# Kernel optimization log

Hardware: AMD Instinct MI355X
Metric: run time of the kernel (lower is better)

## Reference

```python
import jax, jax.numpy as jnp
import numpy as np

N_NODES = 4096
HID = 64
N_STEP = 10
_OFFSETS = np.array([1, 2, 5, 11, 23, 47, 97, 193])  # circulant graph -> degree 16


def setup_inputs() -> dict:
    rng = np.random.default_rng(0)
    N = N_NODES
    i = np.repeat(np.arange(N), len(_OFFSETS))
    j = (i + np.tile(_OFFSETS, N)) % N
    vals = rng.normal(0.0, 0.5, i.shape).astype(np.float32)
    J = np.zeros((N, N), np.float32)
    J[i, j] = vals
    J[j, i] = vals  # symmetric coupling matrix
    row, col = np.nonzero(J)                      # E directed edges, row-major sorted
    key_fwd = row.astype(np.int64) * N + col
    rev = np.searchsorted(key_fwd, col.astype(np.int64) * N + row)  # reverse-edge index
    ru, cu = np.nonzero(np.triu(J))               # Eu upper-triangular edges
    u2e = np.searchsorted(key_fwd, ru.astype(np.int64) * N + cu)    # upper -> full edge index
    bias = rng.normal(0.0, 0.5, N).astype(np.float32)
    p = lambda *s: jnp.asarray(rng.normal(0.0, 0.1, s).astype(np.float32))
    return {
        'J': jnp.asarray(J), 'bias': jnp.asarray(bias),
        'gat_W': p(4, HID), 'gat_a': p(2 * HID, 1),
        'ci_W1': p(4, HID), 'ci_b1': jnp.zeros((HID,), jnp.float32),
        'ci_W2': p(HID, HID), 'ci_b2': jnp.zeros((HID,), jnp.float32),
        'ci_W3': p(HID, 1), 'ci_b3': jnp.zeros((1,), jnp.float32),
        'row': jnp.asarray(row.astype(np.int32)), 'col': jnp.asarray(col.astype(np.int32)),
        'rev': jnp.asarray(rev.astype(np.int32)),
        'ru': jnp.asarray(ru.astype(np.int32)), 'cu': jnp.asarray(cu.astype(np.int32)),
        'u2e': jnp.asarray(u2e.astype(np.int32)),
        'N_step': N_STEP, 'MPNNtype': 0,
    }


def reference(J, bias, gat_W, gat_a, ci_W1, ci_b1, ci_W2, ci_b2, ci_W3, ci_b3,
              row, col, rev, ru, cu, u2e, N_step, MPNNtype):
    N = J.shape[0]
    adj = (jnp.abs(J) > 0).astype(J.dtype)
    # node features: [-b, b, degree, row-sum of J]
    feat = jnp.stack([-bias, bias, adj.sum(1), J.sum(1)], axis=1)  # [N,4]
    # GAT scores: e[i,j] = leakyrelu([Wh_i || Wh_j] @ a) = leakyrelu(Wh_i@a1 + Wh_j@a2)
    Wh = feat @ gat_W                                  # [N,H]
    f1 = Wh @ gat_a[:HID, 0]
    f2 = Wh @ gat_a[HID:, 0]
    e = jax.nn.leaky_relu(f1[:, None] + f2[None, :], 0.2)
    att = jnp.where(adj > 0, jnp.exp(e), 0.0)
    Cij_matrix = 0.5 * (att + att.T)                   # [N,N]
    Cij_e = Cij_matrix[row, col]                       # [E]
    # Ci readout MLP
    h = jax.nn.relu(feat @ ci_W1 + ci_b1)
    h = jax.nn.relu(h @ ci_W2 + ci_b2)
    Ci = h @ ci_W3 + ci_b3                             # [N,1]
    dom = Ci + Cij_matrix.sum(1, keepdims=True)
    dom = jnp.sign(dom) * jnp.maximum(jnp.abs(dom), 0.1)  # clamp |.| >= 0.1
    bias_scale = bias / dom[:, 0]
    bx_scale = jnp.stack([-bias_scale, bias_scale], axis=1)  # [N,2]
    Jv = J[row, col]
    Jxy_scale = jnp.stack([jnp.stack([Jv, -Jv], -1),
                           jnp.stack([-Jv, Jv], -1)], axis=1) / Cij_e[:, None, None]  # [E,2,2]

    def node_update(em):
        # node_messages[j,:] = sum over edges (i->j) of em[e,:]
        nm = jax.ops.segment_sum(em, col, num_segments=N) / dom   # [N,2]
        lnZ = jnp.log(jnp.sum(jnp.exp(bx_scale + nm), axis=1, keepdims=True))
        return bx_scale + nm - lnZ, lnZ

    em0 = jnp.zeros((row.shape[0], 2), J.dtype)  # log of all-ones messages
    hidden0, lnZ0 = node_update(em0)

    def bp_step(carry, _):
        em, hidden, lnZ = carry
        ln_pj = hidden[row][:, :, None]     # [E,2,1]
        ln_zj = lnZ[row][:, :, None]        # [E,1,1]
        ln_mu_ij = em[rev][:, :, None]      # message on reverse edge, [E,2,1]
        M = jnp.exp(Jxy_scale + ln_pj + ln_zj - ln_mu_ij)          # [E,2,2]
        M = M / jnp.sum(jnp.max(M, axis=1), axis=1)[:, None, None]
        em_new = jnp.log(jnp.max(M ** Cij_e[:, None, None], axis=1))  # [E,2]
        hidden_new, lnZ_new = node_update(em_new)
        return (em_new, hidden_new, lnZ_new), None

    (em, hidden, lnZ), _ = jax.lax.scan(bp_step, (em0, hidden0, lnZ0), None, length=N_step)

    readout = jnp.exp(hidden)                           # [N,2]
    Js = J[ru, cu] / Cij_matrix[ru, cu]                 # [Eu]
    Jxy_u = jnp.exp(jnp.stack([jnp.stack([Js, -Js], -1),
                               jnp.stack([-Js, Js], -1)], axis=1))  # [Eu,2,2]
    temp_i = readout[cu] / jnp.exp(em[u2e])             # [Eu,2]
    temp_j = readout[ru] / jnp.exp(em[rev[u2e]])        # [Eu,2]
    pw = Jxy_u * temp_i[:, None, :] * temp_j[:, :, None]
    pw = pw / jnp.sum(pw, axis=(1, 2), keepdims=True)
    readout_pairwise = pw.reshape(-1, 4)                # [Eu,4]
    Cij_u = Cij_matrix[ru, cu]
    node_H = -jnp.sum(readout * jnp.log(readout + 1e-16), axis=1)
    edge_H = -jnp.sum(readout_pairwise * jnp.log(readout_pairwise + 1e-16), axis=1)
    node_entropy = Ci[:, 0] @ jax.lax.stop_gradient(node_H)
    edge_entropy = Cij_u @ jax.lax.stop_gradient(edge_H)
    return (readout, readout_pairwise, node_entropy + edge_entropy,
            node_entropy, edge_entropy, Ci[:, 0], Cij_u, dom)
```

## Files before the change

### kernel.cpp

```cpp
#include <hip/hip_runtime.h>
#include <cstddef>

#define TB    512
#define NB    128
#define NSTEP 10

__device__ __forceinline__ float lse2(float a, float b) {
    return fmaxf(a, b) + __logf(1.0f + __expf(-fabsf(a - b)));
}

__device__ __forceinline__ void stA(float2* p, float2 v) {
    union { float2 f; unsigned long long u; } x; x.f = v;
    __hip_atomic_store((unsigned long long*)p, x.u,
                       __ATOMIC_RELAXED, __HIP_MEMORY_SCOPE_AGENT);
}
__device__ __forceinline__ float2 ldA(const float2* p) {
    union { float2 f; unsigned long long u; } x;
    x.u = __hip_atomic_load((const unsigned long long*)p,
                            __ATOMIC_RELAXED, __HIP_MEMORY_SCOPE_AGENT);
    return x.f;
}

struct KParams {
    const float *J, *bias, *gat_W, *gat_a, *W1, *b1, *W2, *b2, *W3, *b3;
    const int *col, *rev, *ru, *cu, *u2e;
    int N, Eu;
    float2 *jsC, *uA, *uB, *em;
    int*    bar;
    float  *ci_out, *dom_out, *ent;
    float2* ro_out;
    float4* rp_out;
    float*  cij_out;
};

__device__ __forceinline__ void grid_bar(int* flags, int expect) {
    __syncthreads();
    if (threadIdx.x == 0)
        __hip_atomic_store(&flags[blockIdx.x * 32], expect,
                           __ATOMIC_RELAXED, __HIP_MEMORY_SCOPE_AGENT);
    if (threadIdx.x < NB) {
        while (__hip_atomic_load(&flags[threadIdx.x * 32], __ATOMIC_RELAXED,
                                 __HIP_MEMORY_SCOPE_AGENT) < expect) {}
    }
    __syncthreads();
}

__global__ __launch_bounds__(TB) void k_fused(KParams p) {
    __shared__ float sW2[64 * 64];
    __shared__ float sh1[TB / 16][65];
    __shared__ float red[TB / 64];

    const int tidb = threadIdx.x;
    const int g = blockIdx.x * TB + tidb;
    const int i = g >> 4, t = g & 15;
    const int lane = tidb & 63;

    for (int k = tidb; k < 64 * 64; k += TB) sW2[k] = p.W2[k];
    if (g < 3) {
        __hip_atomic_store((int*)&p.ent[g], 0,
                           __ATOMIC_RELAXED, __HIP_MEMORY_SCOPE_AGENT);
    }

    const int j  = p.col[g];
    const float Jv = p.J[(size_t)i * (size_t)p.N + (size_t)j];

    float rs = Jv;
    rs += __shfl_xor(rs, 1); rs += __shfl_xor(rs, 2);
    rs += __shfl_xor(rs, 4); rs += __shfl_xor(rs, 8);

    float rsj = 0.0f;
    {
        const int* colj = p.col + 16 * j;
        const float* Jrow = p.J + (size_t)j * (size_t)p.N;
        #pragma unroll 4
        for (int tt = 0; tt < 16; ++tt) rsj += Jrow[colj[tt]];
    }

    const float bi = p.bias[i], bj = p.bias[j];

    float s8 = 0.0f;
    if (lane < 8) {
        int k = lane & 3;
        const float* a = p.gat_a + ((lane < 4) ? 0 : 64);
        for (int h = 0; h < 64; ++h) s8 += p.gat_W[k * 64 + h] * a[h];
    }
    const float w10 = __shfl(s8, 0), w11 = __shfl(s8, 1), w12 = __shfl(s8, 2), w13 = __shfl(s8, 3);
    const float w20 = __shfl(s8, 4), w21 = __shfl(s8, 5), w22 = __shfl(s8, 6), w23 = __shfl(s8, 7);
    const float fd = 16.0f;
    const float f1i = -bi * w10 + bi * w11 + fd * w12 + rs  * w13;
    const float f2i = -bi * w20 + bi * w21 + fd * w22 + rs  * w23;
    const float f1j = -bj * w10 + bj * w11 + fd * w12 + rsj * w13;
    const float f2j = -bj * w20 + bj * w21 + fd * w22 + rsj * w23;

    float x1 = f1i + f2j; x1 = (x1 > 0.0f) ? x1 : 0.2f * x1;
    float x2 = f1j + f2i; x2 = (x2 > 0.0f) ? x2 : 0.2f * x2;
    const float C  = 0.5f * (__expf(x1) + __expf(x2));
    const float js = Jv / C;
    stA(&p.jsC[g], make_float2(js, C));

    float sc = C;
    sc += __shfl_xor(sc, 1); sc += __shfl_xor(sc, 2);
    sc += __shfl_xor(sc, 4); sc += __shfl_xor(sc, 8);

    const int nib = tidb >> 4;
    __syncthreads();
    #pragma unroll
    for (int m = 0; m < 4; ++m) {
        int h = t + 16 * m;
        float a = -bi * p.W1[h] + bi * p.W1[64 + h] + fd * p.W1[128 + h]
                + rs * p.W1[192 + h] + p.b1[h];
        sh1[nib][h] = fmaxf(a, 0.0f);
    }
    __syncthreads();
    float civ = 0.0f;
    #pragma unroll
    for (int m = 0; m < 4; ++m) {
        int o = t + 16 * m;
        float acc = p.b2[o];
        for (int h = 0; h < 64; ++h) acc += sh1[nib][h] * sW2[h * 64 + o];
        civ += fmaxf(acc, 0.0f) * p.W3[o];
    }
    civ += __shfl_xor(civ, 1); civ += __shfl_xor(civ, 2);
    civ += __shfl_xor(civ, 4); civ += __shfl_xor(civ, 8);
    const float ci = civ + p.b3[0];

    const float s  = ci + sc;
    const float cl = fmaxf(fabsf(s), 0.1f);
    const float d  = (s > 0.0f) ? cl : ((s < 0.0f) ? -cl : 0.0f);
    const float rd = 1.0f / d;
    const float bs = bi * rd;
    if (t == 0) {
        p.ci_out[i] = ci;
        p.dom_out[i] = d;
        stA(&p.uA[i], make_float2(-bs, bs));
    }
    grid_bar(p.bar, 1);

    int eE = 0, eR = 0, eC = 0, eEr = 0;
    float jse = 0.0f, Ce = 0.0f;
    if (g < p.Eu) {
        eE = p.u2e[g]; eR = p.ru[g]; eC = p.cu[g];
        eEr = p.rev[eE];
        const float2 jc = ldA(&p.jsC[eE]);
        jse = jc.x; Ce = jc.y;
    }

    float in0 = 0.0f, in1 = 0.0f;
    float out0 = 0.0f, out1 = 0.0f;
    float ui0 = -bs, ui1 = bs;
    float2 *uP = p.uA, *uQ = p.uB;
    for (int st = 0; st < NSTEP; ++st) {
        const float2 uj = ldA(&uP[j]);
        const float a0 = uj.x - out0, a1 = uj.y - out1;
        const float t0 = fmaxf( js + a0, -js + a1);
        const float t1 = fmaxf(-js + a0,  js + a1);
        const float ls = lse2(t0, t1);
        const float ni0 = C * (t0 - ls), ni1 = C * (t1 - ls);
        const float b0 = ui0 - in0, b1 = ui1 - in1;
        const float q0 = fmaxf( js + b0, -js + b1);
        const float q1 = fmaxf(-js + b0,  js + b1);
        const float qs = lse2(q0, q1);
        out0 = C * (q0 - qs); out1 = C * (q1 - qs);
        in0 = ni0; in1 = ni1;

        float nm0 = in0, nm1 = in1;
        nm0 += __shfl_xor(nm0, 1); nm1 += __shfl_xor(nm1, 1);
        nm0 += __shfl_xor(nm0, 2); nm1 += __shfl_xor(nm1, 2);
        nm0 += __shfl_xor(nm0, 4); nm1 += __shfl_xor(nm1, 4);
        nm0 += __shfl_xor(nm0, 8); nm1 += __shfl_xor(nm1, 8);
        ui0 = -bs + nm0 * rd; ui1 = bs + nm1 * rd;
        if (t == 0) stA(&uQ[i], make_float2(ui0, ui1));

        if (st == NSTEP - 1) {
            stA(&p.em[g], make_float2(in0, in1));
            float nodeC = 0.0f;
            if (t == 0) {
                const float lz = lse2(ui0, ui1);
                const float r0 = __expf(ui0 - lz), r1 = __expf(ui1 - lz);
                p.ro_out[i] = make_float2(r0, r1);
                const float H = -(r0 * __logf(r0 + 1e-16f) + r1 * __logf(r1 + 1e-16f));
                nodeC = ci * H;
            }
            for (int off = 32; off > 0; off >>= 1) nodeC += __shfl_down(nodeC, off);
            const int wv = tidb >> 6;
            if (lane == 0) red[wv] = nodeC;
            __syncthreads();
            if (tidb == 0) {
                float sn = 0.0f;
                #pragma unroll
                for (int w = 0; w < TB / 64; ++w) sn += red[w];
                atomicAdd(&p.ent[0], sn);
                atomicAdd(&p.ent[1], sn);
            }
        }
        grid_bar(p.bar, 2 + st);
        float2* tp = uP; uP = uQ; uQ = tp;
    }

    float edgeC = 0.0f;
    if (g < p.Eu) {
        const float2 uc = ldA(&uP[eC]), ur = ldA(&uP[eR]);
        const float lc = lse2(uc.x, uc.y);
        const float lr = lse2(ur.x, ur.y);
        const float2 eme = ldA(&p.em[eEr]);
        const float2 emr = ldA(&p.em[eE]);
        const float ti0 = (uc.x - lc) - eme.x, ti1 = (uc.y - lc) - eme.y;
        const float tj0 = (ur.x - lr) - emr.x, tj1 = (ur.y - lr) - emr.y;
        const float L00 =  jse + ti0 + tj0;
        const float L01 = -jse + ti1 + tj0;
        const float L10 = -jse + ti0 + tj1;
        const float L11 =  jse + ti1 + tj1;
        const float mL = fmaxf(fmaxf(L00, L01), fmaxf(L10, L11));
        float p00 = __expf(L00 - mL), p01 = __expf(L01 - mL);
        float p10 = __expf(L10 - mL), p11 = __expf(L11 - mL);
        const float inv = 1.0f / (p00 + p01 + p10 + p11);
        p00 *= inv; p01 *= inv; p10 *= inv; p11 *= inv;
        p.rp_out[g] = make_float4(p00, p01, p10, p11);
        p.cij_out[g] = Ce;
        const float H = -(p00 * __logf(p00 + 1e-16f) + p01 * __logf(p01 + 1e-16f)
                        + p10 * __logf(p10 + 1e-16f) + p11 * __logf(p11 + 1e-16f));
        edgeC = Ce * H;
    }
    for (int off = 32; off > 0; off >>= 1) edgeC += __shfl_down(edgeC, off);
    const int wv = tidb >> 6;
    if (lane == 0) red[wv] = edgeC;
    __syncthreads();
    if (tidb == 0) {
        float se = 0.0f;
        #pragma unroll
        for (int w = 0; w < TB / 64; ++w) se += red[w];
        atomicAdd(&p.ent[0], se);
        atomicAdd(&p.ent[2], se);
    }
}

extern "C" void kernel_launch(void* const* d_in, const int* in_sizes, int n_in,
                              void* d_out, int out_size, void* d_ws, size_t ws_size,
                              hipStream_t stream) {
    const int N  = in_sizes[1];
    const int E  = in_sizes[10];
    const int Eu = in_sizes[13];

    float* out = (float*)d_out;
    size_t OFF_RP  = 2 * (size_t)N;
    size_t OFF_ENT = OFF_RP + 4 * (size_t)Eu;

    char* w = (char*)d_ws;
    auto carve = [&](size_t bytes) {
        void* q = (void*)w;
        w += (bytes + 255) & ~(size_t)255;
        return q;
    };

    KParams p;
    p.J     = (const float*)d_in[0];
    p.bias  = (const float*)d_in[1];
    p.gat_W = (const float*)d_in[2];
    p.gat_a = (const float*)d_in[3];
    p.W1    = (const float*)d_in[4];
    p.b1    = (const float*)d_in[5];
    p.W2    = (const float*)d_in[6];
    p.b2    = (const float*)d_in[7];
    p.W3    = (const float*)d_in[8];
    p.b3    = (const float*)d_in[9];
    p.col   = (const int*)d_in[11];
    p.rev   = (const int*)d_in[12];
    p.ru    = (const int*)d_in[13];
    p.cu    = (const int*)d_in[14];
    p.u2e   = (const int*)d_in[15];
    p.N = N; p.Eu = Eu;

    p.jsC   = (float2*)carve((size_t)E * 8);
    p.uA    = (float2*)carve((size_t)N * 8);
    p.uB    = (float2*)carve((size_t)N * 8);
    p.em    = (float2*)carve((size_t)E * 8);
    p.bar   = (int*)carve((size_t)NB * 128);

    p.ro_out  = (float2*)out;
    p.rp_out  = (float4*)(out + OFF_RP);
    p.ent     = out + OFF_ENT;
    p.ci_out  = p.ent + 3;
    p.cij_out = p.ci_out + N;
    p.dom_out = p.cij_out + Eu;

    hipMemsetAsync(p.bar, 0, (size_t)NB * 128, stream);
    k_fused<<<dim3(NB), dim3(TB), 0, stream>>>(p);
}
```

Baseline: 160.4 us.

## Replace grid barriers with per-value sentinel polling and step-indexed buffers

Drops the all-block grid barrier. Each value (node GAT features, jsC, em, per-step messages) is now written to a buffer prefilled with a sentinel (0xFF), and consumers spin until their specific entries become valid. Per-step message buffers are indexed by step so they are never overwritten, which removes the need for double buffering. Neighbour row-sum recomputation is replaced by reading the neighbour's published f1/f2. This adds a memset of about 11*N plus 2*E float2 per call and relies on relaxed atomics holding the ordering between data producers and polling consumers.

```diff
diff --git a/kernel.cpp b/kernel.cpp
--- a/kernel.cpp
+++ b/kernel.cpp
@@ -4,6 +4,7 @@
 #define TB    512
 #define NB    128
 #define NSTEP 10
+#define SENTV 0xFFFFFFFFFFFFFFFFULL
 
 __device__ __forceinline__ float lse2(float a, float b) {
     return fmaxf(a, b) + __logf(1.0f + __expf(-fabsf(a - b)));
@@ -14,10 +15,15 @@
     __hip_atomic_store((unsigned long long*)p, x.u,
                        __ATOMIC_RELAXED, __HIP_MEMORY_SCOPE_AGENT);
 }
-__device__ __forceinline__ float2 ldA(const float2* p) {
+__device__ __forceinline__ float2 pollLd(const float2* p) {
     union { float2 f; unsigned long long u; } x;
     x.u = __hip_atomic_load((const unsigned long long*)p,
                             __ATOMIC_RELAXED, __HIP_MEMORY_SCOPE_AGENT);
+    while (x.u == SENTV) {
+        __builtin_amdgcn_s_sleep(1);
+        x.u = __hip_atomic_load((const unsigned long long*)p,
+                                __ATOMIC_RELAXED, __HIP_MEMORY_SCOPE_AGENT);
+    }
     return x.f;
 }
 
@@ -25,26 +31,13 @@
     const float *J, *bias, *gat_W, *gat_a, *W1, *b1, *W2, *b2, *W3, *b3;
     const int *col, *rev, *ru, *cu, *u2e;
     int N, Eu;
-    float2 *jsC, *uA, *uB, *em;
-    int*    bar;
+    float2 *fA, *jsC, *em, *uS;
     float  *ci_out, *dom_out, *ent;
     float2* ro_out;
     float4* rp_out;
     float*  cij_out;
 };
 
-__device__ __forceinline__ void grid_bar(int* flags, int expect) {
-    __syncthreads();
-    if (threadIdx.x == 0)
-        __hip_atomic_store(&flags[blockIdx.x * 32], expect,
-                           __ATOMIC_RELAXED, __HIP_MEMORY_SCOPE_AGENT);
-    if (threadIdx.x < NB) {
-        while (__hip_atomic_load(&flags[threadIdx.x * 32], __ATOMIC_RELAXED,
-                                 __HIP_MEMORY_SCOPE_AGENT) < expect) {}
-    }
-    __syncthreads();
-}
-
 __global__ __launch_bounds__(TB) void k_fused(KParams p) {
     __shared__ float sW2[64 * 64];
     __shared__ float sh1[TB / 16][65];
@@ -54,6 +47,7 @@
     const int g = blockIdx.x * TB + tidb;
     const int i = g >> 4, t = g & 15;
     const int lane = tidb & 63;
+    const int N = p.N;
 
     for (int k = tidb; k < 64 * 64; k += TB) sW2[k] = p.W2[k];
     if (g < 3) {
@@ -62,21 +56,13 @@
     }
 
     const int j  = p.col[g];
-    const float Jv = p.J[(size_t)i * (size_t)p.N + (size_t)j];
+    const float Jv = p.J[(size_t)i * (size_t)N + (size_t)j];
 
     float rs = Jv;
     rs += __shfl_xor(rs, 1); rs += __shfl_xor(rs, 2);
     rs += __shfl_xor(rs, 4); rs += __shfl_xor(rs, 8);
 
-    float rsj = 0.0f;
-    {
-        const int* colj = p.col + 16 * j;
-        const float* Jrow = p.J + (size_t)j * (size_t)p.N;
-        #pragma unroll 4
-        for (int tt = 0; tt < 16; ++tt) rsj += Jrow[colj[tt]];
-    }
-
-    const float bi = p.bias[i], bj = p.bias[j];
+    const float bi = p.bias[i];
 
     float s8 = 0.0f;
     if (lane < 8) {
@@ -87,20 +73,9 @@
     const float w10 = __shfl(s8, 0), w11 = __shfl(s8, 1), w12 = __shfl(s8, 2), w13 = __shfl(s8, 3);
     const float w20 = __shfl(s8, 4), w21 = __shfl(s8, 5), w22 = __shfl(s8, 6), w23 = __shfl(s8, 7);
     const float fd = 16.0f;
-    const float f1i = -bi * w10 + bi * w11 + fd * w12 + rs  * w13;
-    const float f2i = -bi * w20 + bi * w21 + fd * w22 + rs  * w23;
-    const float f1j = -bj * w10 + bj * w11 + fd * w12 + rsj * w13;
-    const float f2j = -bj * w20 + bj * w21 + fd * w22 + rsj * w23;
-
-    float x1 = f1i + f2j; x1 = (x1 > 0.0f) ? x1 : 0.2f * x1;
-    float x2 = f1j + f2i; x2 = (x2 > 0.0f) ? x2 : 0.2f * x2;
-    const float C  = 0.5f * (__expf(x1) + __expf(x2));
-    const float js = Jv / C;
-    stA(&p.jsC[g], make_float2(js, C));
-
-    float sc = C;
-    sc += __shfl_xor(sc, 1); sc += __shfl_xor(sc, 2);
-    sc += __shfl_xor(sc, 4); sc += __shfl_xor(sc, 8);
+    const float f1i = -bi * w10 + bi * w11 + fd * w12 + rs * w13;
+    const float f2i = -bi * w20 + bi * w21 + fd * w22 + rs * w23;
+    if (t == 0) stA(&p.fA[i], make_float2(f1i, f2i));
 
     const int nib = tidb >> 4;
     __syncthreads();
@@ -124,6 +99,16 @@
     civ += __shfl_xor(civ, 4); civ += __shfl_xor(civ, 8);
     const float ci = civ + p.b3[0];
 
+    const float2 fj = pollLd(&p.fA[j]);
+    float x1 = f1i + fj.y; x1 = (x1 > 0.0f) ? x1 : 0.2f * x1;
+    float x2 = fj.x + f2i; x2 = (x2 > 0.0f) ? x2 : 0.2f * x2;
+    const float C  = 0.5f * (__expf(x1) + __expf(x2));
+    const float js = Jv / C;
+    stA(&p.jsC[g], make_float2(js, C));
+
+    float sc = C;
+    sc += __shfl_xor(sc, 1); sc += __shfl_xor(sc, 2);
+    sc += __shfl_xor(sc, 4); sc += __shfl_xor(sc, 8);
     const float s  = ci + sc;
     const float cl = fmaxf(fabsf(s), 0.1f);
     const float d  = (s > 0.0f) ? cl : ((s < 0.0f) ? -cl : 0.0f);
@@ -132,25 +117,20 @@
     if (t == 0) {
         p.ci_out[i] = ci;
         p.dom_out[i] = d;
-        stA(&p.uA[i], make_float2(-bs, bs));
-    }
-    grid_bar(p.bar, 1);
+        stA(&p.uS[i], make_float2(-bs, bs));
+    }
 
     int eE = 0, eR = 0, eC = 0, eEr = 0;
-    float jse = 0.0f, Ce = 0.0f;
     if (g < p.Eu) {
         eE = p.u2e[g]; eR = p.ru[g]; eC = p.cu[g];
         eEr = p.rev[eE];
-        const float2 jc = ldA(&p.jsC[eE]);
-        jse = jc.x; Ce = jc.y;
     }
 
     float in0 = 0.0f, in1 = 0.0f;
     float out0 = 0.0f, out1 = 0.0f;
     float ui0 = -bs, ui1 = bs;
-    float2 *uP = p.uA, *uQ = p.uB;
     for (int st = 0; st < NSTEP; ++st) {
-        const float2 uj = ldA(&uP[j]);
+        const float2 uj = pollLd(&p.uS[(size_t)st * N + j]);
         const float a0 = uj.x - out0, a1 = uj.y - out1;
         const float t0 = fmaxf( js + a0, -js + a1);
         const float t1 = fmaxf(-js + a0,  js + a1);
@@ -169,41 +149,43 @@
         nm0 += __shfl_xor(nm0, 4); nm1 += __shfl_xor(nm1, 4);
         nm0 += __shfl_xor(nm0, 8); nm1 += __shfl_xor(nm1, 8);
         ui0 = -bs + nm0 * rd; ui1 = bs + nm1 * rd;
-        if (t == 0) stA(&uQ[i], make_float2(ui0, ui1));
-
-        if (st == NSTEP - 1) {
-            stA(&p.em[g], make_float2(in0, in1));
-            float nodeC = 0.0f;
-            if (t == 0) {
-                const float lz = lse2(ui0, ui1);
-                const float r0 = __expf(ui0 - lz), r1 = __expf(ui1 - lz);
-                p.ro_out[i] = make_float2(r0, r1);
-                const float H = -(r0 * __logf(r0 + 1e-16f) + r1 * __logf(r1 + 1e-16f));
-                nodeC = ci * H;
-            }
-            for (int off = 32; off > 0; off >>= 1) nodeC += __shfl_down(nodeC, off);
-            const int wv = tidb >> 6;
-            if (lane == 0) red[wv] = nodeC;
-            __syncthreads();
-            if (tidb == 0) {
-                float sn = 0.0f;
-                #pragma unroll
-                for (int w = 0; w < TB / 64; ++w) sn += red[w];
-                atomicAdd(&p.ent[0], sn);
-                atomicAdd(&p.ent[1], sn);
-            }
+        if (t == 0) stA(&p.uS[(size_t)(st + 1) * N + i], make_float2(ui0, ui1));
+        if (st == NSTEP - 1) stA(&p.em[g], make_float2(in0, in1));
+    }
+
+    float nodeC = 0.0f;
+    if (t == 0) {
+        const float lz = lse2(ui0, ui1);
+        const float r0 = __expf(ui0 - lz), r1 = __expf(ui1 - lz);
+        p.ro_out[i] = make_float2(r0, r1);
+        const float H = -(r0 * __logf(r0 + 1e-16f) + r1 * __logf(r1 + 1e-16f));
+        nodeC = ci * H;
+    }
+    for (int off = 32; off > 0; off >>= 1) nodeC += __shfl_down(nodeC, off);
+    {
+        const int wv = tidb >> 6;
+        if (lane == 0) red[wv] = nodeC;
+        __syncthreads();
+        if (tidb == 0) {
+            float sn = 0.0f;
+            #pragma unroll
+            for (int w = 0; w < TB / 64; ++w) sn += red[w];
+            atomicAdd(&p.ent[0], sn);
+            atomicAdd(&p.ent[1], sn);
         }
-        grid_bar(p.bar, 2 + st);
-        float2* tp = uP; uP = uQ; uQ = tp;
-    }
-
+        __syncthreads();
+    }
+
+    const float2* uF = p.uS + (size_t)NSTEP * N;
     float edgeC = 0.0f;
     if (g < p.Eu) {
-        const float2 uc = ldA(&uP[eC]), ur = ldA(&uP[eR]);
+        const float2 jc = pollLd(&p.jsC[eE]);
+        const float jse = jc.x, Ce = jc.y;
+        const float2 uc = pollLd(&uF[eC]), ur = pollLd(&uF[eR]);
+        const float2 eme = pollLd(&p.em[eEr]);
+        const float2 emr = pollLd(&p.em[eE]);
         const float lc = lse2(uc.x, uc.y);
         const float lr = lse2(ur.x, ur.y);
-        const float2 eme = ldA(&p.em[eEr]);
-        const float2 emr = ldA(&p.em[eE]);
         const float ti0 = (uc.x - lc) - eme.x, ti1 = (uc.y - lc) - eme.y;
         const float tj0 = (ur.x - lr) - emr.x, tj1 = (ur.y - lr) - emr.y;
         const float L00 =  jse + ti0 + tj0;
@@ -270,11 +252,14 @@
     p.u2e   = (const int*)d_in[15];
     p.N = N; p.Eu = Eu;
 
-    p.jsC   = (float2*)carve((size_t)E * 8);
-    p.uA    = (float2*)carve((size_t)N * 8);
-    p.uB    = (float2*)carve((size_t)N * 8);
-    p.em    = (float2*)carve((size_t)E * 8);
-    p.bar   = (int*)carve((size_t)NB * 128);
+    const size_t szFA = (size_t)N * 8;
+    const size_t szJC = (size_t)E * 8;
+    const size_t szEM = (size_t)E * 8;
+    const size_t szUS = (size_t)(NSTEP + 1) * N * 8;
+    p.fA  = (float2*)carve(szFA);
+    p.jsC = (float2*)carve(szJC);
+    p.em  = (float2*)carve(szEM);
+    p.uS  = (float2*)carve(szUS);
 
     p.ro_out  = (float2*)out;
     p.rp_out  = (float4*)(out + OFF_RP);
@@ -283,6 +268,6 @@
     p.cij_out = p.ci_out + N;
     p.dom_out = p.cij_out + Eu;
 
-    hipMemsetAsync(p.bar, 0, (size_t)NB * 128, stream);
+    hipMemsetAsync(p.fA, 0xFF, szFA + szJC + szEM + szUS, stream);
     k_fused<<<dim3(NB), dim3(TB), 0, stream>>>(p);
 }
```

New measurement: 157.2 us. 2.0% less time.
